# Optimization experiments

Measured on AMD Instinct MI355X. Metric: run time of the kernel, lower is better.

Reference implementation:

```python
import jax, jax.numpy as jnp
import numpy as np

B, N, K, D, H, L = 2, 2048, 256, 768, 256, 64
REL_PROP = 3
NUM_BUCKETS = 64


def _pair_scores(u, dist_feat, left_w, left_b, right_w, right_b, out_w, out_b):
    # OptFFpairs-style pairwise scorer: left(u)_i + right(u)_j + dist_emb -> relu -> out
    left = jnp.einsum('bkd,hd->bkh', u, left_w) + left_b    # [B,K,H]
    right = jnp.einsum('bkd,hd->bkh', u, right_w) + right_b  # [B,K,H]
    h = jax.nn.relu(left[:, :, None, :] + right[:, None, :, :] + dist_feat)  # [B,K,K,H]
    return jnp.einsum('bijh,lh->bijl', h, out_w) + out_b     # [B,K,K,L]


def setup_inputs():
    key = jax.random.key(0)
    ks = jax.random.split(key, 12)
    s = 0.02
    all_span_vecs = jax.random.normal(ks[0], (B, N, D), dtype=jnp.float32)
    span_vecs = jax.random.normal(ks[1], (B, K, D), dtype=jnp.float32)
    span_begin = jnp.sort(jax.random.randint(ks[2], (B, K), 0, 1000), axis=-1).astype(jnp.int32)
    span_end = (span_begin + jax.random.randint(ks[3], (B, K), 1, 16)).astype(jnp.int32)
    square_mask = jnp.ones((B, K, K), dtype=jnp.float32)
    span_lengths = jnp.full((B,), float(K), dtype=jnp.float32)
    prune_indices = jnp.stack([
        jnp.sort(jax.random.choice(jax.random.fold_in(ks[4], b), N, (K,), replace=False))
        for b in range(B)
    ]).astype(jnp.int32)
    return {
        'all_span_vecs': all_span_vecs, 'span_vecs': span_vecs,
        'span_begin': span_begin, 'span_end': span_end,
        'square_mask': square_mask, 'span_lengths': span_lengths,
        'prune_indices': prune_indices,
        'left_w': jax.random.normal(ks[5], (H, D)) * s, 'left_b': jnp.zeros((H,), jnp.float32),
        'right_w': jax.random.normal(ks[6], (H, D)) * s, 'right_b': jnp.zeros((H,), jnp.float32),
        'dist_emb': jax.random.normal(ks[7], (NUM_BUCKETS, H)) * s,
        'out_w': jax.random.normal(ks[8], (L, H)) * s, 'out_b': jnp.zeros((L,), jnp.float32),
        'A_w': jax.random.normal(ks[9], (D, L)) * s,
        'B_w': jax.random.normal(ks[10], (D, L)) * s,
        'gate_w': jax.random.normal(ks[11], (D, 2 * D)) * s, 'gate_b': jnp.zeros((D,), jnp.float32),
    }


def reference(all_span_vecs, span_vecs, span_begin, span_end, square_mask, span_lengths,
              prune_indices, left_w, left_b, right_w, right_b, dist_emb, out_w, out_b,
              A_w, B_w, gate_w, gate_b):
    # distance-bucket embedding of the span pair (span_pair_generator)
    dist = span_begin[:, None, :] - span_end[:, :, None]                 # [B,K,K]
    buckets = jnp.clip(jnp.abs(dist), 0, NUM_BUCKETS - 1)
    dist_feat = dist_emb[buckets]                                        # [B,K,K,H]
    inv_len = 1.0 / span_lengths[:, None, None]                          # [B,1,1]

    update = span_vecs
    scores = _pair_scores(update, dist_feat, left_w, left_b, right_w, right_b, out_w, out_b)
    for _ in range(REL_PROP):
        probs = jax.nn.sigmoid(scores) * square_mask[..., None]          # [B,K,K,L]
        # torch: (A(probs) * update.unsqueeze(-2)).sum(-3) -> sum over i (rows)
        ctxt1 = jnp.einsum('bijl,dl,bid->bjd', probs, A_w, update) * inv_len
        # torch: (B(probs) * update.unsqueeze(-3)).sum(-2) -> sum over j (cols)
        ctxt2 = jnp.einsum('bijl,dl,bjd->bid', probs, B_w, update) * inv_len
        c = ctxt1 + ctxt2
        # MyGate: sigmoid-gated convex combination of old state and context
        g = jax.nn.sigmoid(jnp.concatenate([update, c], axis=-1) @ gate_w.T + gate_b)
        update = g * update + (1.0 - g) * c
        scores = _pair_scores(update, dist_feat, left_w, left_b, right_w, right_b, out_w, out_b)

    # overwrite_spans: scatter updated filtered spans back into the full span tensor
    valid = jnp.arange(K)[None, :] < span_lengths[:, None]               # [B,K]
    old = jnp.take_along_axis(all_span_vecs, prune_indices[..., None], axis=1)
    vals = jnp.where(valid[..., None], update, old)
    bidx = jnp.arange(B)[:, None]
    new_all = all_span_vecs.at[bidx, prune_indices].set(vals)
    return new_all, update, scores
```

## Files before the change

### kernel.cpp

```cpp
#include <hip/hip_runtime.h>

#define B_ 2
#define N_ 2048
#define K_ 256
#define D_ 768
#define H_ 256
#define L_ 64
#define BK_ (B_*K_)

typedef __attribute__((ext_vector_type(8))) __bf16 bf16x8;
typedef __attribute__((ext_vector_type(8))) unsigned short ushort8;
typedef __attribute__((ext_vector_type(4))) unsigned short ushort4v;
typedef __attribute__((ext_vector_type(4))) float f32x4;

__device__ __forceinline__ float sigm(float x) { return 1.0f / (1.0f + __expf(-x)); }

__device__ __forceinline__ unsigned short f2b(float f) {
    union { float f; unsigned int u; } v; v.f = f;
    unsigned int u = v.u;
    return (unsigned short)((u + 0x7FFFu + ((u >> 16) & 1u)) >> 16);
}
__device__ __forceinline__ unsigned short f2bc(float f) {
    __bf16 h = (__bf16)f;
    return __builtin_bit_cast(unsigned short, h);
}
__device__ __forceinline__ float b2f(unsigned short us) {
    union { unsigned int u; float f; } v; v.u = ((unsigned int)us) << 16;
    return v.f;
}
__device__ __forceinline__ bf16x8 ldb(const unsigned short* p) {
    ushort8 v = *(const ushort8*)p;
    return __builtin_bit_cast(bf16x8, v);
}

__global__ __launch_bounds__(256) void conv_all(
    const float* __restrict__ lw, const float* __restrict__ rw,
    const float* __restrict__ ow, const float* __restrict__ gw,
    const float* __restrict__ aw, const float* __restrict__ bw,
    const float* __restrict__ sv,
    unsigned short* __restrict__ lwb, unsigned short* __restrict__ rwb,
    unsigned short* __restrict__ owb, unsigned short* __restrict__ gwb,
    unsigned short* __restrict__ wab, unsigned short* __restrict__ wbb,
    unsigned short* __restrict__ ub)
{
    int i4 = (blockIdx.x * 256 + threadIdx.x) * 4;
    const float* src; unsigned short* dst; int off;
    if      (i4 <  196608) { src = lw; dst = lwb; off = 0; }
    else if (i4 <  393216) { src = rw; dst = rwb; off = 196608; }
    else if (i4 <  409600) { src = ow; dst = owb; off = 393216; }
    else if (i4 < 1589248) { src = gw; dst = gwb; off = 409600; }
    else if (i4 < 1638400) { src = aw; dst = wab; off = 1589248; }
    else if (i4 < 1687552) { src = bw; dst = wbb; off = 1638400; }
    else if (i4 < 2080768) { src = sv; dst = ub;  off = 1687552; }
    else return;
    int j = i4 - off;
    float4 v = *(const float4*)&src[j];
    ushort4v p; p.x = f2b(v.x); p.y = f2b(v.y); p.z = f2b(v.z); p.w = f2b(v.w);
    *(ushort4v*)&dst[j] = p;
}

__global__ __launch_bounds__(256) void conv_c(
    const float* __restrict__ c, unsigned short* __restrict__ cb)
{
    int i = (blockIdx.x * 256 + threadIdx.x) * 4;
    float4 v = *(const float4*)&c[i];
    ushort4v p; p.x = f2b(v.x); p.y = f2b(v.y); p.z = f2b(v.z); p.w = f2b(v.w);
    *(ushort4v*)&cb[i] = p;
}

__global__ __launch_bounds__(64) void lr_mfma2(
    const unsigned short* __restrict__ Ub,
    const unsigned short* __restrict__ lwb, const float* __restrict__ lb,
    const unsigned short* __restrict__ rwb, const float* __restrict__ rb,
    float* __restrict__ outL, float* __restrict__ outR)
{
    const int side = blockIdx.z;
    const unsigned short* __restrict__ W = side ? rwb : lwb;
    const float* __restrict__ bias = side ? rb : lb;
    float* __restrict__ outp = side ? outR : outL;
    const int r0 = blockIdx.x * 16, n0 = blockIdx.y * 16;
    const int lane = threadIdx.x;
    const int col = lane & 15, quad = lane >> 4;
    const unsigned short* arow = &Ub[(size_t)(r0 + col)*D_ + quad*8];
    const unsigned short* brow = &W[(size_t)(n0 + col)*D_ + quad*8];
    f32x4 acc = {};
    #pragma unroll
    for (int kc = 0; kc < D_; kc += 32) {
        bf16x8 a = ldb(arow + kc);
        bf16x8 bb = ldb(brow + kc);
        acc = __builtin_amdgcn_mfma_f32_16x16x32_bf16(a, bb, acc, 0, 0, 0);
    }
    const int n = n0 + col;
    const float bv = bias[n];
    #pragma unroll
    for (int r = 0; r < 4; ++r)
        outp[(size_t)(r0 + quad*4 + r)*H_ + n] = acc[r] + bv;
}

__global__ __launch_bounds__(256) void scores_v11(
    const float* __restrict__ leftb, const float* __restrict__ rightb,
    const int* __restrict__ span_begin, const int* __restrict__ span_end,
    const float* __restrict__ de, const unsigned short* __restrict__ owb,
    const float* __restrict__ out_b, const float* __restrict__ mask,
    float* __restrict__ S, unsigned short* __restrict__ Pt,
    unsigned short* __restrict__ Pt2, int writeP)
{
    const int j0 = blockIdx.x * 64;
    const int i0 = blockIdx.y * 4;
    const int b  = blockIdx.z;
    const int tid = threadIdx.x;
    const int w = tid >> 6, lane = tid & 63, col = lane & 15, quad = lane >> 4;
    const int jrow = w*16 + col;

    __shared__ float sL[4][256];
    __shared__ float sT[64][68];
    __shared__ float sMask[4][64];
    __shared__ int   sBkt[4][64];

    {
        int ii = tid >> 6, jj = tid & 63;
        int d = span_begin[b*K_ + j0 + jj] - span_end[b*K_ + i0 + ii];
        if (d < 0) d = -d;
        sBkt[ii][jj] = d > 63 ? 63 : d;
        sMask[ii][jj] = mask[(size_t)(b*K_ + i0 + ii)*K_ + j0 + jj];
    }
    {
        int row = tid >> 6, c4 = (tid & 63) * 4;
        *(float4*)&sL[row][c4] = *(const float4*)&leftb[(size_t)(b*K_ + i0 + row)*H_ + c4];
    }
    __syncthreads();

    int deoff[4];
    #pragma unroll
    for (int i = 0; i < 4; ++i) deoff[i] = sBkt[i][jrow] * H_;

    const float* rrow = &rightb[(size_t)(b*K_ + j0 + jrow)*H_ + quad*8];

    f32x4 acc[4][4] = {};
    #pragma unroll
    for (int k = 0; k < 8; ++k) {
        const float4 r0 = *(const float4*)&rrow[k*32];
        const float4 r1 = *(const float4*)&rrow[k*32 + 4];
        bf16x8 bbk[4];
        #pragma unroll
        for (int lt = 0; lt < 4; ++lt)
            bbk[lt] = ldb(&owb[(size_t)(lt*16 + col)*H_ + k*32 + quad*8]);
        #pragma unroll
        for (int i = 0; i < 4; ++i) {
            const float* dr = &de[deoff[i] + k*32 + quad*8];
            const float4 d0 = *(const float4*)dr;
            const float4 d1 = *(const float4*)(dr + 4);
            const float* lr = &sL[i][k*32 + quad*8];
            const float4 l0 = *(const float4*)lr;
            const float4 l1 = *(const float4*)(lr + 4);
            bf16x8 a;
            a[0] = (__bf16)fmaxf(0.f, l0.x + r0.x + d0.x);
            a[1] = (__bf16)fmaxf(0.f, l0.y + r0.y + d0.y);
            a[2] = (__bf16)fmaxf(0.f, l0.z + r0.z + d0.z);
            a[3] = (__bf16)fmaxf(0.f, l0.w + r0.w + d0.w);
            a[4] = (__bf16)fmaxf(0.f, l1.x + r1.x + d1.x);
            a[5] = (__bf16)fmaxf(0.f, l1.y + r1.y + d1.y);
            a[6] = (__bf16)fmaxf(0.f, l1.z + r1.z + d1.z);
            a[7] = (__bf16)fmaxf(0.f, l1.w + r1.w + d1.w);
            #pragma unroll
            for (int lt = 0; lt < 4; ++lt)
                acc[i][lt] = __builtin_amdgcn_mfma_f32_16x16x32_bf16(a, bbk[lt], acc[i][lt], 0, 0, 0);
        }
    }

    float ob[4];
    #pragma unroll
    for (int lt = 0; lt < 4; ++lt) ob[lt] = out_b[lt*16 + col];

    #pragma unroll
    for (int i = 0; i < 4; ++i) {
        __syncthreads();
        #pragma unroll
        for (int lt = 0; lt < 4; ++lt)
            #pragma unroll
            for (int r = 0; r < 4; ++r)
                sT[w*16 + quad*4 + r][lt*16 + col] = acc[i][lt][r] + ob[lt];
        __syncthreads();
        const int jj = tid >> 2, seg = (tid & 3) * 16;
        const int j = j0 + jj, ii = i0 + i;
        if (writeP) {
            const float msk = sMask[i][jj];
            ushort8 o0, o1;
            #pragma unroll
            for (int e = 0; e < 8; ++e) {
                o0[e] = f2bc(sigm(sT[jj][seg + e]) * msk);
                o1[e] = f2bc(sigm(sT[jj][seg + 8 + e]) * msk);
            }
            unsigned short* dst = &Pt[(((size_t)b*K_ + j)*K_ + ii)*L_ + seg];
            *(ushort8*)&dst[0] = o0;
            *(ushort8*)&dst[8] = o1;
            unsigned short* dst2 = &Pt2[(((size_t)b*K_ + ii)*K_ + j)*L_ + seg];
            *(ushort8*)&dst2[0] = o0;
            *(ushort8*)&dst2[8] = o1;
        } else {
            float* dst = &S[(((size_t)b*K_ + ii)*K_ + j)*L_ + seg];
            #pragma unroll
            for (int q2 = 0; q2 < 4; ++q2) {
                float4 v;
                v.x = sT[jj][seg + q2*4 + 0];
                v.y = sT[jj][seg + q2*4 + 1];
                v.z = sT[jj][seg + q2*4 + 2];
                v.w = sT[jj][seg + q2*4 + 3];
                *(float4*)&dst[q2*4] = v;
            }
        }
    }
}

__global__ __launch_bounds__(512, 4) void ctxt_v8(
    const unsigned short* __restrict__ Pt, const unsigned short* __restrict__ Pt2,
    const float* __restrict__ U,
    const unsigned short* __restrict__ WAb, const unsigned short* __restrict__ WBb,
    const float* __restrict__ lens, float* __restrict__ cacc)
{
    const int bid = blockIdx.x;
    const int m0 = (bid & 15) << 4;
    const int t0 = ((bid >> 4) & 7) << 5;
    const int mode = (bid >> 7) & 1;
    const int b = bid >> 8;
    const unsigned short* __restrict__ Wb    = mode ? WBb : WAb;
    const unsigned short* __restrict__ Pbase = mode ? Pt  : Pt2;
    const int tid = threadIdx.x;
    const int w = tid >> 6, lane = tid & 63, col = lane & 15, quad = lane >> 4;
    const int dbase = w * 96;

    bf16x8 bw[6][2];
    #pragma unroll
    for (int dt = 0; dt < 6; ++dt)
        #pragma unroll
        for (int kc = 0; kc < 2; ++kc)
            bw[dt][kc] = ldb(&Wb[(size_t)(dbase + dt*16 + col)*L_ + kc*32 + quad*8]);

    const size_t fragoff = (size_t)col*L_ + quad*8;
    f32x4 acc[6] = {};
    #pragma unroll 2
    for (int t = 0; t < 32; ++t) {
        const unsigned short* pA =
            &Pbase[(((size_t)(b*K_ + t0 + t))*K_ + m0)*L_];
        bf16x8 a0 = ldb(&pA[fragoff]);
        bf16x8 a1 = ldb(&pA[fragoff + 32]);
        const float* urow = &U[(size_t)(b*K_ + t0 + t)*D_ + dbase + col];
        #pragma unroll
        for (int dt = 0; dt < 6; ++dt) {
            f32x4 g = {0.f, 0.f, 0.f, 0.f};
            g = __builtin_amdgcn_mfma_f32_16x16x32_bf16(a0, bw[dt][0], g, 0, 0, 0);
            g = __builtin_amdgcn_mfma_f32_16x16x32_bf16(a1, bw[dt][1], g, 0, 0, 0);
            acc[dt] += g * urow[dt*16];
        }
    }

    const float inv_len = 1.0f / lens[b];
    #pragma unroll
    for (int dt = 0; dt < 6; ++dt)
        #pragma unroll
        for (int r = 0; r < 4; ++r) {
            const int m = m0 + quad*4 + r;
            atomicAdd(&cacc[((size_t)(b*K_) + m)*D_ + dbase + dt*16 + col],
                      acc[dt][r] * inv_len);
        }
}

__global__ __launch_bounds__(64) void gate_mfma2(
    const unsigned short* __restrict__ Ub, const unsigned short* __restrict__ cb,
    const unsigned short* __restrict__ gwb, const float* __restrict__ gb,
    const float* __restrict__ Ucur, const float* __restrict__ Cc,
    float* __restrict__ Unext, unsigned short* __restrict__ Ubnext)
{
    const int r0 = blockIdx.x * 16, n0 = blockIdx.y * 16;
    const int lane = threadIdx.x;
    const int col = lane & 15, quad = lane >> 4;
    const unsigned short* arow_u = &Ub[(size_t)(r0 + col)*D_ + quad*8];
    const unsigned short* arow_c = &cb[(size_t)(r0 + col)*D_ + quad*8];
    const unsigned short* brow   = &gwb[(size_t)(n0 + col)*(2*D_) + quad*8];
    f32x4 acc = {};
    #pragma unroll
    for (int kc = 0; kc < D_; kc += 32) {
        bf16x8 a = ldb(arow_u + kc);
        bf16x8 bb = ldb(brow + kc);
        acc = __builtin_amdgcn_mfma_f32_16x16x32_bf16(a, bb, acc, 0, 0, 0);
    }
    #pragma unroll
    for (int kc = 0; kc < D_; kc += 32) {
        bf16x8 a = ldb(arow_c + kc);
        bf16x8 bb = ldb(brow + D_ + kc);
        acc = __builtin_amdgcn_mfma_f32_16x16x32_bf16(a, bb, acc, 0, 0, 0);
    }
    const int n = n0 + col;
    const float gbv = gb[n];
    #pragma unroll
    for (int r = 0; r < 4; ++r) {
        const size_t idx = (size_t)(r0 + quad*4 + r)*D_ + n;
        const float gg = sigm(acc[r] + gbv);
        const float o = gg * Ucur[idx] + (1.f - gg) * Cc[idx];
        Unext[idx] = o;
        Ubnext[idx] = f2b(o);
    }
}

__global__ __launch_bounds__(256) void scatter_kernel(
    const float* __restrict__ upd, const int* __restrict__ prune,
    const float* __restrict__ lens, float* __restrict__ out_all)
{
    const int blk = blockIdx.x;
    const int b = blk / K_, k = blk % K_;
    if ((float)k < lens[b]) {
        const int pi = prune[b*K_ + k];
        const int tid = threadIdx.x;
        if (tid < D_/4) {
            float4 v = *(const float4*)&upd[((size_t)b*K_ + k)*D_ + tid*4];
            *(float4*)&out_all[((size_t)b*N_ + pi)*D_ + tid*4] = v;
        }
    }
}

extern "C" void kernel_launch(void* const* d_in, const int* in_sizes, int n_in,
                              void* d_out, int out_size, void* d_ws, size_t ws_size,
                              hipStream_t stream) {
    (void)in_sizes; (void)n_in; (void)out_size; (void)ws_size;
    const float* all_span_vecs = (const float*)d_in[0];
    const float* span_vecs     = (const float*)d_in[1];
    const int*   span_begin    = (const int*)d_in[2];
    const int*   span_end      = (const int*)d_in[3];
    const float* mask          = (const float*)d_in[4];
    const float* lens          = (const float*)d_in[5];
    const int*   prune         = (const int*)d_in[6];
    const float* lw  = (const float*)d_in[7];
    const float* lb  = (const float*)d_in[8];
    const float* rw  = (const float*)d_in[9];
    const float* rb  = (const float*)d_in[10];
    const float* dist_emb = (const float*)d_in[11];
    const float* out_w    = (const float*)d_in[12];
    const float* out_b    = (const float*)d_in[13];
    const float* A_w = (const float*)d_in[14];
    const float* B_w = (const float*)d_in[15];
    const float* gw  = (const float*)d_in[16];
    const float* gb  = (const float*)d_in[17];

    float* out_all = (float*)d_out;
    float* out_upd = out_all + (size_t)B_*N_*D_;
    float* out_sc  = out_upd + (size_t)BK_*D_;

    float* ws     = (float*)d_ws;
    float* leftb  = ws;
    float* rightf = leftb + (size_t)BK_*H_;
    float* U0     = rightf + (size_t)BK_*H_;
    float* U1     = U0 + (size_t)BK_*D_;
    float* cbuf   = U1 + (size_t)BK_*D_;
    unsigned short* WAb = (unsigned short*)(cbuf + (size_t)BK_*D_);
    unsigned short* WBb = WAb + (size_t)D_*L_;
    unsigned short* lwb = WBb + (size_t)D_*L_;
    unsigned short* rwb = lwb + (size_t)H_*D_;
    unsigned short* owb = rwb + (size_t)H_*D_;
    unsigned short* gwb = owb + (size_t)L_*H_;
    unsigned short* Ub0 = gwb + (size_t)D_*2*D_;
    unsigned short* Ub1 = Ub0 + (size_t)BK_*D_;
    unsigned short* cb  = Ub1 + (size_t)BK_*D_;
    unsigned short* Pt  = cb + (size_t)BK_*D_;
    unsigned short* Pt2 = Pt + (size_t)B_*K_*K_*L_;

    hipMemcpyAsync(out_all, all_span_vecs, sizeof(float)*(size_t)B_*N_*D_,
                   hipMemcpyDeviceToDevice, stream);

    dim3 blk256(256), blk64(64), blk512(512);
    conv_all<<<dim3(2032), blk256, 0, stream>>>(lw, rw, out_w, gw, A_w, B_w, span_vecs,
                                                lwb, rwb, owb, gwb, WAb, WBb, Ub0);
    lr_mfma2<<<dim3(BK_/16, H_/16, 2), blk64, 0, stream>>>(Ub0, lwb, lb, rwb, rb, leftb, rightf);
    scores_v11<<<dim3(K_/64, K_/4, B_), blk256, 0, stream>>>(leftb, rightf, span_begin, span_end,
                                                             dist_emb, owb, out_b, mask,
                                                             out_sc, Pt, Pt2, 1);
    const float* Ucur = span_vecs;
    const unsigned short* Ubcur = Ub0;
    float* nexts[3] = {U0, U1, out_upd};
    unsigned short* nextsUb[3] = {Ub1, Ub0, Ub1};
    for (int it = 0; it < 3; ++it) {
        hipMemsetAsync(cbuf, 0, sizeof(float)*(size_t)BK_*D_, stream);
        ctxt_v8<<<dim3(512), blk512, 0, stream>>>(Pt, Pt2, Ucur, WAb, WBb, lens, cbuf);
        conv_c<<<dim3(BK_*D_/1024), blk256, 0, stream>>>(cbuf, cb);
        gate_mfma2<<<dim3(BK_/16, D_/16), blk64, 0, stream>>>(Ubcur, cb, gwb, gb,
                                                              Ucur, cbuf, nexts[it], nextsUb[it]);
        Ucur = nexts[it];
        Ubcur = nextsUb[it];
        lr_mfma2<<<dim3(BK_/16, H_/16, 2), blk64, 0, stream>>>(Ubcur, lwb, lb, rwb, rb, leftb, rightf);
        scores_v11<<<dim3(K_/64, K_/4, B_), blk256, 0, stream>>>(leftb, rightf, span_begin, span_end,
                                                                 dist_emb, owb, out_b, mask,
                                                                 out_sc, Pt, Pt2, it == 2 ? 0 : 1);
    }
    scatter_kernel<<<dim3(BK_), blk256, 0, stream>>>(out_upd, prune, lens, out_all);
}
```

Baseline: 535.3 us.

## Replace atomic context accumulation with partial-sum slots and deterministic reduce

The context kernel now writes per-(mode, t-block) partial sums into 16 separate slots and no longer uses atomicAdd into a zeroed buffer. A new reduce kernel sums the slots and also emits the bf16 copy, which drops the memset and the separate conversion kernel. The update matrix is transposed into a per-batch [D,K] layout each iteration so each thread loads four consecutive t values as a float4. This costs a 16x larger workspace buffer, more global traffic in the reduction, an extra transpose launch per iteration, and a lower occupancy hint.

New measurement: 511.1 us. 4.5% less time.

```diff
diff --git a/kernel.cpp b/kernel.cpp
--- a/kernel.cpp
+++ b/kernel.cpp
@@ -59,13 +59,35 @@
     *(ushort4v*)&dst[j] = p;
 }
 
-__global__ __launch_bounds__(256) void conv_c(
-    const float* __restrict__ c, unsigned short* __restrict__ cb)
-{
-    int i = (blockIdx.x * 256 + threadIdx.x) * 4;
-    float4 v = *(const float4*)&c[i];
-    ushort4v p; p.x = f2b(v.x); p.y = f2b(v.y); p.z = f2b(v.z); p.w = f2b(v.w);
-    *(ushort4v*)&cb[i] = p;
+__global__ __launch_bounds__(256) void ut_kernel(
+    const float* __restrict__ U, float* __restrict__ Ut)
+{
+    __shared__ float tile[32][33];
+    const int kb = blockIdx.x * 32, db = blockIdx.y * 32, b = blockIdx.z;
+    const int tx = threadIdx.x & 31, ty = threadIdx.x >> 5;
+    #pragma unroll
+    for (int r = 0; r < 32; r += 8)
+        tile[r + ty][tx] = U[(size_t)(b*K_ + kb + r + ty)*D_ + db + tx];
+    __syncthreads();
+    #pragma unroll
+    for (int r = 0; r < 32; r += 8)
+        Ut[(size_t)(b*D_ + db + r + ty)*K_ + kb + tx] = tile[tx][r + ty];
+}
+
+__global__ __launch_bounds__(256) void reduce_c(
+    const float* __restrict__ part, float* __restrict__ cbuf,
+    unsigned short* __restrict__ cb)
+{
+    const size_t i4 = ((size_t)blockIdx.x * 256 + threadIdx.x) * 4;
+    float4 s = {0.f, 0.f, 0.f, 0.f};
+    #pragma unroll
+    for (int sl = 0; sl < 16; ++sl) {
+        float4 v = *(const float4*)&part[(size_t)sl*BK_*D_ + i4];
+        s.x += v.x; s.y += v.y; s.z += v.z; s.w += v.w;
+    }
+    *(float4*)&cbuf[i4] = s;
+    ushort4v p; p.x = f2b(s.x); p.y = f2b(s.y); p.z = f2b(s.z); p.w = f2b(s.w);
+    *(ushort4v*)&cb[i4] = p;
 }
 
 __global__ __launch_bounds__(64) void lr_mfma2(
@@ -212,15 +234,16 @@
     }
 }
 
-__global__ __launch_bounds__(512, 4) void ctxt_v8(
+__global__ __launch_bounds__(512, 2) void ctxt_v9(
     const unsigned short* __restrict__ Pt, const unsigned short* __restrict__ Pt2,
-    const float* __restrict__ U,
+    const float* __restrict__ Ut,
     const unsigned short* __restrict__ WAb, const unsigned short* __restrict__ WBb,
-    const float* __restrict__ lens, float* __restrict__ cacc)
+    const float* __restrict__ lens, float* __restrict__ part)
 {
     const int bid = blockIdx.x;
     const int m0 = (bid & 15) << 4;
-    const int t0 = ((bid >> 4) & 7) << 5;
+    const int tblk = (bid >> 4) & 7;
+    const int t0 = tblk << 5;
     const int mode = (bid >> 7) & 1;
     const int b = bid >> 8;
     const unsigned short* __restrict__ Wb    = mode ? WBb : WAb;
@@ -237,32 +260,42 @@
             bw[dt][kc] = ldb(&Wb[(size_t)(dbase + dt*16 + col)*L_ + kc*32 + quad*8]);
 
     const size_t fragoff = (size_t)col*L_ + quad*8;
+    const float* utbase = &Ut[((size_t)b*D_ + dbase + col)*K_ + t0];
+
     f32x4 acc[6] = {};
     #pragma unroll 2
-    for (int t = 0; t < 32; ++t) {
-        const unsigned short* pA =
-            &Pbase[(((size_t)(b*K_ + t0 + t))*K_ + m0)*L_];
-        bf16x8 a0 = ldb(&pA[fragoff]);
-        bf16x8 a1 = ldb(&pA[fragoff + 32]);
-        const float* urow = &U[(size_t)(b*K_ + t0 + t)*D_ + dbase + col];
-        #pragma unroll
-        for (int dt = 0; dt < 6; ++dt) {
-            f32x4 g = {0.f, 0.f, 0.f, 0.f};
-            g = __builtin_amdgcn_mfma_f32_16x16x32_bf16(a0, bw[dt][0], g, 0, 0, 0);
-            g = __builtin_amdgcn_mfma_f32_16x16x32_bf16(a1, bw[dt][1], g, 0, 0, 0);
-            acc[dt] += g * urow[dt*16];
+    for (int tq = 0; tq < 8; ++tq) {
+        float4 uq[6];
+        #pragma unroll
+        for (int dt = 0; dt < 6; ++dt)
+            uq[dt] = *(const float4*)&utbase[(size_t)dt*16*K_ + tq*4];
+        #pragma unroll
+        for (int tt = 0; tt < 4; ++tt) {
+            const int t = tq*4 + tt;
+            const unsigned short* pA =
+                &Pbase[(((size_t)(b*K_ + t0 + t))*K_ + m0)*L_];
+            bf16x8 a0 = ldb(&pA[fragoff]);
+            bf16x8 a1 = ldb(&pA[fragoff + 32]);
+            #pragma unroll
+            for (int dt = 0; dt < 6; ++dt) {
+                f32x4 g = {0.f, 0.f, 0.f, 0.f};
+                g = __builtin_amdgcn_mfma_f32_16x16x32_bf16(a0, bw[dt][0], g, 0, 0, 0);
+                g = __builtin_amdgcn_mfma_f32_16x16x32_bf16(a1, bw[dt][1], g, 0, 0, 0);
+                const float uu = (tt == 0) ? uq[dt].x : (tt == 1) ? uq[dt].y
+                               : (tt == 2) ? uq[dt].z : uq[dt].w;
+                acc[dt] += g * uu;
+            }
         }
     }
 
     const float inv_len = 1.0f / lens[b];
+    const int slot = mode*8 + tblk;
+    float* pout = &part[(((size_t)slot*B_ + b)*K_ + m0)*D_];
     #pragma unroll
     for (int dt = 0; dt < 6; ++dt)
         #pragma unroll
-        for (int r = 0; r < 4; ++r) {
-            const int m = m0 + quad*4 + r;
-            atomicAdd(&cacc[((size_t)(b*K_) + m)*D_ + dbase + dt*16 + col],
-                      acc[dt][r] * inv_len);
-        }
+        for (int r = 0; r < 4; ++r)
+            pout[(size_t)(quad*4 + r)*D_ + dbase + dt*16 + col] = acc[dt][r] * inv_len;
 }
 
 __global__ __launch_bounds__(64) void gate_mfma2(
@@ -351,7 +384,9 @@
     float* U0     = rightf + (size_t)BK_*H_;
     float* U1     = U0 + (size_t)BK_*D_;
     float* cbuf   = U1 + (size_t)BK_*D_;
-    unsigned short* WAb = (unsigned short*)(cbuf + (size_t)BK_*D_);
+    float* Utb    = cbuf + (size_t)BK_*D_;
+    float* part   = Utb + (size_t)BK_*D_;
+    unsigned short* WAb = (unsigned short*)(part + (size_t)16*BK_*D_);
     unsigned short* WBb = WAb + (size_t)D_*L_;
     unsigned short* lwb = WBb + (size_t)D_*L_;
     unsigned short* rwb = lwb + (size_t)H_*D_;
@@ -367,24 +402,27 @@
                    hipMemcpyDeviceToDevice, stream);
 
     dim3 blk256(256), blk64(64), blk512(512);
+    dim3 utgrid(K_/32, D_/32, B_);
     conv_all<<<dim3(2032), blk256, 0, stream>>>(lw, rw, out_w, gw, A_w, B_w, span_vecs,
                                                 lwb, rwb, owb, gwb, WAb, WBb, Ub0);
     lr_mfma2<<<dim3(BK_/16, H_/16, 2), blk64, 0, stream>>>(Ub0, lwb, lb, rwb, rb, leftb, rightf);
     scores_v11<<<dim3(K_/64, K_/4, B_), blk256, 0, stream>>>(leftb, rightf, span_begin, span_end,
                                                              dist_emb, owb, out_b, mask,
                                                              out_sc, Pt, Pt2, 1);
+    ut_kernel<<<utgrid, blk256, 0, stream>>>(span_vecs, Utb);
     const float* Ucur = span_vecs;
     const unsigned short* Ubcur = Ub0;
     float* nexts[3] = {U0, U1, out_upd};
     unsigned short* nextsUb[3] = {Ub1, Ub0, Ub1};
     for (int it = 0; it < 3; ++it) {
-        hipMemsetAsync(cbuf, 0, sizeof(float)*(size_t)BK_*D_, stream);
-        ctxt_v8<<<dim3(512), blk512, 0, stream>>>(Pt, Pt2, Ucur, WAb, WBb, lens, cbuf);
-        conv_c<<<dim3(BK_*D_/1024), blk256, 0, stream>>>(cbuf, cb);
+        ctxt_v9<<<dim3(512), blk512, 0, stream>>>(Pt, Pt2, Utb, WAb, WBb, lens, part);
+        reduce_c<<<dim3(BK_*D_/1024), blk256, 0, stream>>>(part, cbuf, cb);
         gate_mfma2<<<dim3(BK_/16, D_/16), blk64, 0, stream>>>(Ubcur, cb, gwb, gb,
                                                               Ucur, cbuf, nexts[it], nextsUb[it]);
         Ucur = nexts[it];
         Ubcur = nextsUb[it];
+        if (it < 2)
+            ut_kernel<<<utgrid, blk256, 0, stream>>>(Ucur, Utb);
         lr_mfma2<<<dim3(BK_/16, H_/16, 2), blk64, 0, stream>>>(Ubcur, lwb, lb, rwb, rb, leftb, rightf);
         scores_v11<<<dim3(K_/64, K_/4, B_), blk256, 0, stream>>>(leftb, rightf, span_begin, span_end,
                                                                  dist_emb, owb, out_b, mask,
```
